# Optimization experiments

Hardware: AMD Instinct MI355X
Metric: run time of the kernel (lower is better)

Reference implementation:

```python
import jax, jax.numpy as jnp
import numpy as np

L, M, K, H, F, D = 8, 32768, 8, 128, 32, 3  # fronts, nodes/front, in-degree, hidden, feat, depth-branches


def _resnet(x, w1, b1, w2, b2, w3, b3):
    # resnet module: lay3(tanh(lay2(tanh(lay1(x)))) + x)
    h1 = jnp.tanh(x @ w1 + b1)
    h2 = jnp.tanh(h1 @ w2 + b2)
    return (h2 + x) @ w3 + b3


def setup_inputs() -> dict:
    key = jax.random.key(0)
    ks = iter(jax.random.split(key, 80))

    def nrm(shape, fan_in):
        return jax.random.normal(next(ks), shape, jnp.float32) / np.float32(np.sqrt(fan_in))

    def bias(shape):
        return 0.01 * jax.random.normal(next(ks), shape, jnp.float32)

    inp = {}
    inp["node_feats"] = jax.random.normal(next(ks), (L, M, F), jnp.float32)
    inp["pred_idx"] = jax.random.randint(next(ks), (L - 1, M, K), 0, M, jnp.int32)
    inp["embed_w"] = nrm((F, H), F); inp["embed_b"] = bias((H,))
    # d{1,2,3}_mp_bwd and d{1,2,3}_mp_bwd1 : per-depth pair of H-resnets, stacked [D,2,...]
    inp["mp_w1"] = nrm((D, 2, H, H), H); inp["mp_b1"] = bias((D, 2, H))
    inp["mp_w2"] = nrm((D, 2, H, H), H); inp["mp_b2"] = bias((D, 2, H))
    inp["mp_w3"] = nrm((D, 2, H, H), H); inp["mp_b3"] = bias((D, 2, H))
    for p in ("comb", "node"):  # d*_comb_embed(+1), d*_node_embeds(+1)
        inp[p + "_wide_w1"] = nrm((D, 2 * H, 2 * H), 2 * H); inp[p + "_wide_b1"] = bias((D, 2 * H))
        inp[p + "_wide_w2"] = nrm((D, 2 * H, 2 * H), 2 * H); inp[p + "_wide_b2"] = bias((D, 2 * H))
        inp[p + "_wide_w3"] = nrm((D, 2 * H, H), 2 * H);     inp[p + "_wide_b3"] = bias((D, H))
        inp[p + "_h_w1"] = nrm((D, H, H), H); inp[p + "_h_b1"] = bias((D, H))
        inp[p + "_h_w2"] = nrm((D, H, H), H); inp[p + "_h_b2"] = bias((D, H))
        inp[p + "_h_w3"] = nrm((D, H, H), H); inp[p + "_h_b3"] = bias((D, H))
    return inp


def reference(node_feats, pred_idx, embed_w, embed_b,
              mp_w1, mp_b1, mp_w2, mp_b2, mp_w3, mp_b3,
              comb_wide_w1, comb_wide_b1, comb_wide_w2, comb_wide_b2, comb_wide_w3, comb_wide_b3,
              comb_h_w1, comb_h_b1, comb_h_w2, comb_h_b2, comb_h_w3, comb_h_b3,
              node_wide_w1, node_wide_b1, node_wide_w2, node_wide_b2, node_wide_w3, node_wide_b3,
              node_h_w1, node_h_b1, node_h_w2, node_h_b2, node_h_w3, node_h_b3):
    # front 0 (topological roots): apply_func only -> tanh(embed_op(feats))
    e = jnp.tanh(node_feats[0] @ embed_w + embed_b)          # [M, H]
    outs = [e]
    prev = e
    for l in range(1, L):
        d = min(l - 1, 2)                                    # bwd_depth branch (d1/d2/d3)
        # msg_func + redux_func: gather mailbox from predecessor front, sum-reduce, MLP
        s = prev[pred_idx[l - 1]].sum(axis=1)                # [M, K, H] -> [M, H]
        r = jnp.tanh(_resnet(s, mp_w1[d, 0], mp_b1[d, 0], mp_w2[d, 0], mp_b2[d, 0], mp_w3[d, 0], mp_b3[d, 0]))
        r = jnp.tanh(_resnet(r, mp_w1[d, 1], mp_b1[d, 1], mp_w2[d, 1], mp_b2[d, 1], mp_w3[d, 1], mp_b3[d, 1]))
        # apply_func: embed, comb branch (bwd_node_embeds is all-zero for not-yet-processed nodes),
        # then node_embeds branch on cat(embeds, msgs_redux)
        e = jnp.tanh(node_feats[l] @ embed_w + embed_b)
        c = jnp.concatenate([e, jnp.zeros_like(e)], axis=-1)  # [M, 2H]
        e = jnp.tanh(_resnet(c, comb_wide_w1[d], comb_wide_b1[d], comb_wide_w2[d], comb_wide_b2[d], comb_wide_w3[d], comb_wide_b3[d]))
        e = jnp.tanh(_resnet(e, comb_h_w1[d], comb_h_b1[d], comb_h_w2[d], comb_h_b2[d], comb_h_w3[d], comb_h_b3[d]))
        c2 = jnp.concatenate([e, r], axis=-1)                 # [M, 2H]
        e = jnp.tanh(_resnet(c2, node_wide_w1[d], node_wide_b1[d], node_wide_w2[d], node_wide_b2[d], node_wide_w3[d], node_wide_b3[d]))
        e = jnp.tanh(_resnet(e, node_h_w1[d], node_h_b1[d], node_h_w2[d], node_h_b2[d], node_h_w3[d], node_h_b3[d]))
        outs.append(e)
        prev = e
    return jnp.stack(outs)                                    # graph.ndata['bwd_node_embeds'] : [L, M, H]
```

## Files before the change

kernel.cpp:

```cpp
#include <hip/hip_runtime.h>
#include <hip/hip_bf16.h>

#define M_NODES 32768

using f16x8 = __attribute__((ext_vector_type(8))) _Float16;
using f16x4 = __attribute__((ext_vector_type(4))) _Float16;
using f32x4 = __attribute__((ext_vector_type(4))) float;
typedef unsigned short u16;
typedef unsigned int   u32;

__device__ __forceinline__ u16 f2h(float f){
  _Float16 h = (_Float16)f;
  return __builtin_bit_cast(u16, h);
}
__device__ __forceinline__ float h2f(u16 h){
  return (float)__builtin_bit_cast(_Float16, h);
}
__device__ __forceinline__ float tanh_fast(float x){
  float t = __builtin_amdgcn_exp2f(x * 2.8853900817779268f);
  return 1.0f - 2.0f * __builtin_amdgcn_rcpf(t + 1.0f);
}

struct PrepPtrs { const float* p[16]; };

__global__ void prep_kernel(PrepPtrs pp, u16* ws){
  const int Bc[16] = {1,6,6,6,3,3,3,3,3,3,3,3,3,3,3,3};
  const int Kc[16] = {32,128,128,128,256,256,256,128,128,128,256,256,256,128,128,128};
  const int Nc[16] = {128,128,128,128,256,256,128,128,128,128,256,256,128,128,128,128};
  const int tot = 1576960;
  for (int i = blockIdx.x*blockDim.x + threadIdx.x; i < tot; i += gridDim.x*blockDim.x){
    int e = i, s = 0;
    while (true){ int sz = Bc[s]*Kc[s]*Nc[s]; if (e < sz) break; e -= sz; ++s; }
    int K = Kc[s], N = Nc[s];
    int kn = K*N;
    int b = e / kn; int r2 = e - b*kn;
    int n = r2 / K; int k = r2 - n*K;
    float v = pp.p[s][(size_t)b*kn + (size_t)k*N + n];
    ws[i] = f2h(v);
  }
}

__global__ __launch_bounds__(256) void front0_kernel(const float* __restrict__ feats,
                                                     const float* __restrict__ ew,
                                                     const float* __restrict__ eb,
                                                     float* __restrict__ out){
  __shared__ float fl[2048];
  const int brow = blockIdx.x * 64;
  const float* f0 = feats + (size_t)brow*32;
#pragma unroll
  for (int it = 0; it < 2; ++it){
    int idx = threadIdx.x + it*256;
    *(float4*)(&fl[idx*4]) = *(const float4*)(f0 + idx*4);
  }
  __syncthreads();
  const int col = threadIdx.x & 127, rh = threadIdx.x >> 7;
  float w[32];
#pragma unroll
  for (int k = 0; k < 32; ++k) w[k] = ew[k*128 + col];
  const float bv = eb[col];
  for (int r = 0; r < 32; ++r){
    int row = rh*32 + r;
    float acc = bv;
#pragma unroll
    for (int k = 0; k < 32; ++k) acc += fl[row*32 + k] * w[k];
    out[(size_t)(brow + row)*128 + col] = tanh_fast(acc);
  }
}

template<int KLOOP, int N, int WS, int AMODE, int RESMODE, int OUTMODE, bool INPLACE>
__device__ __forceinline__ void mm_stage(const u16* inA, u16* outB, const u16* resB,
                                         const u16* __restrict__ wt,
                                         const float* __restrict__ bias,
                                         float* gout, int phase)
{
  const int tid  = threadIdx.x;
  const int lane = tid & 63, nq = tid >> 6;
  const int q = lane >> 4, c = lane & 15;
  constexpr int NT = N / 64;
  constexpr int NP = KLOOP / 32;
  const float* inAf = (const float*)inA;
  float*       outF = (float*)outB;
  const float* resF = (const float*)resB;
  const int msk = NP - 1;
  const int ph = phase & msk;

  const u16* wrow[NT];
#pragma unroll
  for (int j = 0; j < NT; ++j){
    int nt = nq*2 + (j & 1) + (j >> 1) * 8;
    wrow[j] = wt + (size_t)(nt*16 + c)*WS + q*8;
  }
  f16x8 breg[2][NT];
#pragma unroll
  for (int j = 0; j < NT; ++j) breg[0][j] = *(const f16x8*)(wrow[j] + ph*32);
#pragma unroll
  for (int j = 0; j < NT; ++j) breg[1][j] = *(const f16x8*)(wrow[j] + ((ph + 1) & msk)*32);

  f32x4 acc[4][NT];
#pragma unroll
  for (int m = 0; m < 4; ++m)
#pragma unroll
    for (int j = 0; j < NT; ++j) acc[m][j] = (f32x4){0.f,0.f,0.f,0.f};

#pragma unroll
  for (int kp = 0; kp < NP; ++kp){
    const int slot = kp & 1;
    const int kpp = (ph + kp) & msk;
    f16x8 bc[NT];
#pragma unroll
    for (int j = 0; j < NT; ++j) bc[j] = breg[slot][j];
    if (kp + 2 < NP){
      int kn = (ph + kp + 2) & msk;
#pragma unroll
      for (int j = 0; j < NT; ++j) breg[slot][j] = *(const f16x8*)(wrow[j] + kn*32);
    }
#pragma unroll
    for (int m = 0; m < 4; ++m){
      if (AMODE == 0){
        f16x8 af = *(const f16x8*)(&inA[(m*16 + c)*264 + kpp*32 + q*8]);
#pragma unroll
        for (int j = 0; j < NT; ++j)
          acc[m][j] = __builtin_amdgcn_mfma_f32_16x16x32_f16(bc[j], af, acc[m][j], 0, 0, 0);
      } else {
        const float* ap = inAf + (m*16 + c)*132 + kpp*32 + q*8;
        float4 x0 = *(const float4*)(ap);
        float4 x1 = *(const float4*)(ap + 4);
        float xs[8] = {x0.x,x0.y,x0.z,x0.w,x1.x,x1.y,x1.z,x1.w};
        f16x8 ah, al;
#pragma unroll
        for (int k = 0; k < 8; ++k){
          _Float16 hi = (_Float16)xs[k];
          ah[k] = hi;
          al[k] = (_Float16)(xs[k] - (float)hi);
        }
#pragma unroll
        for (int j = 0; j < NT; ++j){
          acc[m][j] = __builtin_amdgcn_mfma_f32_16x16x32_f16(bc[j], ah, acc[m][j], 0, 0, 0);
          acc[m][j] = __builtin_amdgcn_mfma_f32_16x16x32_f16(bc[j], al, acc[m][j], 0, 0, 0);
        }
      }
    }
  }
  if (INPLACE) __syncthreads();
#pragma unroll
  for (int j = 0; j < NT; ++j){
    int nt = nq*2 + (j & 1) + (j >> 1) * 8;
    int col0 = nt*16 + q*4;
    float4 bq = *(const float4*)(bias + col0);
    float bvv[4] = {bq.x, bq.y, bq.z, bq.w};
#pragma unroll
    for (int m = 0; m < 4; ++m){
      int row = m*16 + c;
      float v[4];
#pragma unroll
      for (int r = 0; r < 4; ++r) v[r] = tanh_fast(acc[m][j][r] + bvv[r]);
      if (RESMODE == 2 || (RESMODE == 1 && j < 2)){
        f16x4 rv = *(const f16x4*)(&resB[row*264 + col0]);
#pragma unroll
        for (int r = 0; r < 4; ++r) v[r] += (float)rv[r];
      } else if (RESMODE == 3){
        float4 rf = *(const float4*)(&resF[row*132 + col0]);
        v[0] += rf.x; v[1] += rf.y; v[2] += rf.z; v[3] += rf.w;
      }
      if (OUTMODE == 2){
        float4 o = {v[0], v[1], v[2], v[3]};
        *(float4*)(&gout[(size_t)row*128 + col0]) = o;
      } else if (OUTMODE == 1){
        float4 o = {v[0], v[1], v[2], v[3]};
        *(float4*)(&outF[row*132 + col0]) = o;
      } else {
        f16x4 h;
#pragma unroll
        for (int r = 0; r < 4; ++r) h[r] = (_Float16)v[r];
        *(f16x4*)(&outB[row*264 + col0]) = h;
      }
    }
  }
  __syncthreads();
}

__device__ __forceinline__ void embed_stage(const float* __restrict__ featsRow,
                                            u16* outB, const u16* __restrict__ wt,
                                            const float* __restrict__ bias)
{
  const int tid  = threadIdx.x;
  const int lane = tid & 63, nq = tid >> 6;
  const int q = lane >> 4, c = lane & 15;
  f16x8 bf[2];
#pragma unroll
  for (int j = 0; j < 2; ++j){
    int nt = nq*2 + j;
    bf[j] = *(const f16x8*)(wt + (nt*16 + c)*32 + q*8);
  }
  f32x4 acc[4][2];
#pragma unroll
  for (int m = 0; m < 4; ++m){ acc[m][0] = (f32x4){0,0,0,0}; acc[m][1] = (f32x4){0,0,0,0}; }
#pragma unroll
  for (int m = 0; m < 4; ++m){
    int row = m*16 + c;
    const float* fp = featsRow + (size_t)row*32 + q*8;
    float4 a0 = *(const float4*)(fp);
    float4 a1 = *(const float4*)(fp + 4);
    float xs[8] = {a0.x,a0.y,a0.z,a0.w,a1.x,a1.y,a1.z,a1.w};
    f16x8 ah, al;
#pragma unroll
    for (int k = 0; k < 8; ++k){
      _Float16 hi = (_Float16)xs[k];
      ah[k] = hi;
      al[k] = (_Float16)(xs[k] - (float)hi);
    }
#pragma unroll
    for (int j = 0; j < 2; ++j){
      acc[m][j] = __builtin_amdgcn_mfma_f32_16x16x32_f16(bf[j], ah, acc[m][j], 0, 0, 0);
      acc[m][j] = __builtin_amdgcn_mfma_f32_16x16x32_f16(bf[j], al, acc[m][j], 0, 0, 0);
    }
  }
#pragma unroll
  for (int j = 0; j < 2; ++j){
    int nt = nq*2 + j;
    int col0 = nt*16 + q*4;
    float4 bq = *(const float4*)(bias + col0);
    float bvv[4] = {bq.x, bq.y, bq.z, bq.w};
#pragma unroll
    for (int m = 0; m < 4; ++m){
      int row = m*16 + c;
      f16x4 h;
#pragma unroll
      for (int r = 0; r < 4; ++r) h[r] = (_Float16)tanh_fast(acc[m][j][r] + bvv[r]);
      *(f16x4*)(&outB[row*264 + col0]) = h;
    }
  }
  __syncthreads();
}

struct FrontArgs {
  const float* feats; const int* pred;
  const u16* ws;
  float* out;
  const float* embed_b;
  const float* mp_b1; const float* mp_b2; const float* mp_b3;
  const float* cw_b1; const float* cw_b2; const float* cw_b3;
  const float* ch_b1; const float* ch_b2; const float* ch_b3;
  const float* nw_b1; const float* nw_b2; const float* nw_b3;
  const float* nh_b1; const float* nh_b2; const float* nh_b3;
  int l, d;
};

__global__ __launch_bounds__(256, 2) void front_kernel(FrontArgs A)
{
  extern __shared__ u16 lds[];
  u16* P  = lds;
  u16* Q  = lds + 16896;
  const int brow = blockIdx.x * 64;
  const int d = A.d;
  const u16* ws = A.ws;
  const int ph = blockIdx.x;

  {
    float* Pf = (float*)P;
    const float* prev = A.out + (size_t)(A.l - 1) * M_NODES * 128;
    const int c4 = threadIdx.x & 31;
    const int r0 = threadIdx.x >> 5;
#pragma unroll
    for (int rr = 0; rr < 8; ++rr){
      int row = r0 + rr*8;
      const int* ip = A.pred + ((size_t)(A.l - 1) * M_NODES + brow + row) * 8;
      float sx=0.f, sy=0.f, sz=0.f, sw=0.f;
#pragma unroll
      for (int p = 0; p < 8; ++p){
        const float4 v = *(const float4*)(prev + (size_t)ip[p]*128 + c4*4);
        sx += v.x; sy += v.y; sz += v.z; sw += v.w;
      }
      float4 o = {sx, sy, sz, sw};
      *(float4*)(&Pf[row*132 + c4*4]) = o;
    }
  }
  __syncthreads();

  const int d0 = d*2, d1 = d*2 + 1;
  mm_stage<128,128,128, 1,0,0,false>(P, Q, nullptr, ws + 4096   + (size_t)d0*16384, A.mp_b1 + d0*128, nullptr, ph);
  mm_stage<128,128,128, 0,3,1,false>(Q, P, P,       ws + 102400 + (size_t)d0*16384, A.mp_b2 + d0*128, nullptr, ph);
  mm_stage<128,128,128, 1,0,0,false>(P, Q, nullptr, ws + 200704 + (size_t)d0*16384, A.mp_b3 + d0*128, nullptr, ph);
  mm_stage<128,128,128, 0,0,0,false>(Q, P, nullptr, ws + 4096   + (size_t)d1*16384, A.mp_b1 + d1*128, nullptr, ph);
  mm_stage<128,128,128, 0,2,1,true >(P, P, Q,       ws + 102400 + (size_t)d1*16384, A.mp_b2 + d1*128, nullptr, ph);
  mm_stage<128,128,128, 1,0,0,false>(P, Q + 128, nullptr, ws + 200704 + (size_t)d1*16384, A.mp_b3 + d1*128, nullptr, ph);
  embed_stage(A.feats + ((size_t)A.l * M_NODES + brow) * 32, Q, ws, A.embed_b);
  mm_stage<128,256,256, 0,0,0,false>(Q, P, nullptr, ws + 299008 + (size_t)d*65536, A.cw_b1 + d*256, nullptr, ph);
  mm_stage<256,256,256, 0,1,0,true >(P, P, Q,       ws + 495616 + (size_t)d*65536, A.cw_b2 + d*256, nullptr, ph);
  mm_stage<256,128,256, 0,0,0,false>(P, Q, nullptr, ws + 692224 + (size_t)d*32768, A.cw_b3 + d*128, nullptr, ph);
  mm_stage<128,128,128, 0,0,0,false>(Q, P, nullptr, ws + 790528 + (size_t)d*16384, A.ch_b1 + d*128, nullptr, ph);
  mm_stage<128,128,128, 0,2,0,true >(P, P, Q,       ws + 839680 + (size_t)d*16384, A.ch_b2 + d*128, nullptr, ph);
  mm_stage<128,128,128, 0,0,0,false>(P, Q, nullptr, ws + 888832 + (size_t)d*16384, A.ch_b3 + d*128, nullptr, ph);
  mm_stage<256,256,256, 0,0,0,false>(Q, P, nullptr, ws + 937984  + (size_t)d*65536, A.nw_b1 + d*256, nullptr, ph);
  mm_stage<256,256,256, 0,2,0,true >(P, P, Q,       ws + 1134592 + (size_t)d*65536, A.nw_b2 + d*256, nullptr, ph);
  mm_stage<256,128,256, 0,0,0,false>(P, Q, nullptr, ws + 1331200 + (size_t)d*32768, A.nw_b3 + d*128, nullptr, ph);
  mm_stage<128,128,128, 0,0,0,false>(Q, P, nullptr, ws + 1429504 + (size_t)d*16384, A.nh_b1 + d*128, nullptr, ph);
  mm_stage<128,128,128, 0,2,0,true >(P, P, Q,       ws + 1478656 + (size_t)d*16384, A.nh_b2 + d*128, nullptr, ph);
  float* gout = A.out + ((size_t)A.l * M_NODES + brow) * 128;
  mm_stage<128,128,128, 0,0,2,false>(P, nullptr, nullptr, ws + 1527808 + (size_t)d*16384, A.nh_b3 + d*128, gout, ph);
}

extern "C" void kernel_launch(void* const* d_in, const int* in_sizes, int n_in,
                              void* d_out, int out_size, void* d_ws, size_t ws_size,
                              hipStream_t stream)
{
  (void)in_sizes; (void)n_in; (void)out_size; (void)ws_size;
  const float* feats = (const float*)d_in[0];
  const int*   pred  = (const int*)d_in[1];
  u16*   ws  = (u16*)d_ws;
  float* out = (float*)d_out;

  PrepPtrs pp;
  const int wIdx[16] = {2,4,6,8,10,12,14,16,18,20,22,24,26,28,30,32};
  for (int i = 0; i < 16; ++i) pp.p[i] = (const float*)d_in[wIdx[i]];
  prep_kernel<<<2048, 256, 0, stream>>>(pp, ws);

  front0_kernel<<<M_NODES/64, 256, 0, stream>>>(feats, (const float*)d_in[2], (const float*)d_in[3], out);

  const size_t LDSB = (size_t)(2*64*264) * sizeof(u16);
  (void)hipFuncSetAttribute((const void*)front_kernel,
                            hipFuncAttributeMaxDynamicSharedMemorySize, (int)LDSB);

  FrontArgs A;
  A.feats = feats; A.pred = pred; A.ws = ws; A.out = out;
  A.embed_b = (const float*)d_in[3];
  A.mp_b1 = (const float*)d_in[5];  A.mp_b2 = (const float*)d_in[7];  A.mp_b3 = (const float*)d_in[9];
  A.cw_b1 = (const float*)d_in[11]; A.cw_b2 = (const float*)d_in[13]; A.cw_b3 = (const float*)d_in[15];
  A.ch_b1 = (const float*)d_in[17]; A.ch_b2 = (const float*)d_in[19]; A.ch_b3 = (const float*)d_in[21];
  A.nw_b1 = (const float*)d_in[23]; A.nw_b2 = (const float*)d_in[25]; A.nw_b3 = (const float*)d_in[27];
  A.nh_b1 = (const float*)d_in[29]; A.nh_b2 = (const float*)d_in[31]; A.nh_b3 = (const float*)d_in[33];

  for (int l = 1; l < 8; ++l){
    A.l = l;
    A.d = (l - 1 < 2) ? (l - 1) : 2;
    front_kernel<<<M_NODES/64, 256, LDSB, stream>>>(A);
  }
}
```

Measured before the change: 662.7 us.

## Double threads per block to eight waves, halving per-wave column tiles

Each 64-row tile in front_kernel is now processed by 512 threads instead of 256. Every wave owns half as many 16-column N-tiles in each matmul stage and in the embed stage, and the gather loop covers rows with a stride of 16. The goal is more waves per CU to hide latency, with fewer accumulator registers per thread. The cost is that each weight fragment is loaded by more waves, each wave does less MFMA work between barriers, and the __launch_bounds__(512,4) request may not be met given the LDS use of about 67KB per block.

New measurement: 679.4 us. 2.5% more time.

```diff
diff --git a/kernel.cpp b/kernel.cpp
--- a/kernel.cpp
+++ b/kernel.cpp
@@ -76,7 +76,7 @@
   const int tid  = threadIdx.x;
   const int lane = tid & 63, nq = tid >> 6;
   const int q = lane >> 4, c = lane & 15;
-  constexpr int NT = N / 64;
+  constexpr int NT = N / 128;
   constexpr int NP = KLOOP / 32;
   const float* inAf = (const float*)inA;
   float*       outF = (float*)outB;
@@ -87,7 +87,7 @@
   const u16* wrow[NT];
 #pragma unroll
   for (int j = 0; j < NT; ++j){
-    int nt = nq*2 + (j & 1) + (j >> 1) * 8;
+    int nt = nq + j*8;
     wrow[j] = wt + (size_t)(nt*16 + c)*WS + q*8;
   }
   f16x8 breg[2][NT];
@@ -144,7 +144,7 @@
   if (INPLACE) __syncthreads();
 #pragma unroll
   for (int j = 0; j < NT; ++j){
-    int nt = nq*2 + (j & 1) + (j >> 1) * 8;
+    int nt = nq + j*8;
     int col0 = nt*16 + q*4;
     float4 bq = *(const float4*)(bias + col0);
     float bvv[4] = {bq.x, bq.y, bq.z, bq.w};
@@ -154,7 +154,7 @@
       float v[4];
 #pragma unroll
       for (int r = 0; r < 4; ++r) v[r] = tanh_fast(acc[m][j][r] + bvv[r]);
-      if (RESMODE == 2 || (RESMODE == 1 && j < 2)){
+      if (RESMODE == 2 || (RESMODE == 1 && j == 0)){
         f16x4 rv = *(const f16x4*)(&resB[row*264 + col0]);
 #pragma unroll
         for (int r = 0; r < 4; ++r) v[r] += (float)rv[r];
@@ -186,15 +186,10 @@
   const int tid  = threadIdx.x;
   const int lane = tid & 63, nq = tid >> 6;
   const int q = lane >> 4, c = lane & 15;
-  f16x8 bf[2];
-#pragma unroll
-  for (int j = 0; j < 2; ++j){
-    int nt = nq*2 + j;
-    bf[j] = *(const f16x8*)(wt + (nt*16 + c)*32 + q*8);
-  }
-  f32x4 acc[4][2];
-#pragma unroll
-  for (int m = 0; m < 4; ++m){ acc[m][0] = (f32x4){0,0,0,0}; acc[m][1] = (f32x4){0,0,0,0}; }
+  f16x8 bf = *(const f16x8*)(wt + (nq*16 + c)*32 + q*8);
+  f32x4 acc[4];
+#pragma unroll
+  for (int m = 0; m < 4; ++m) acc[m] = (f32x4){0,0,0,0};
 #pragma unroll
   for (int m = 0; m < 4; ++m){
     int row = m*16 + c;
@@ -209,26 +204,19 @@
       ah[k] = hi;
       al[k] = (_Float16)(xs[k] - (float)hi);
     }
-#pragma unroll
-    for (int j = 0; j < 2; ++j){
-      acc[m][j] = __builtin_amdgcn_mfma_f32_16x16x32_f16(bf[j], ah, acc[m][j], 0, 0, 0);
-      acc[m][j] = __builtin_amdgcn_mfma_f32_16x16x32_f16(bf[j], al, acc[m][j], 0, 0, 0);
-    }
-  }
-#pragma unroll
-  for (int j = 0; j < 2; ++j){
-    int nt = nq*2 + j;
-    int col0 = nt*16 + q*4;
-    float4 bq = *(const float4*)(bias + col0);
-    float bvv[4] = {bq.x, bq.y, bq.z, bq.w};
-#pragma unroll
-    for (int m = 0; m < 4; ++m){
-      int row = m*16 + c;
-      f16x4 h;
-#pragma unroll
-      for (int r = 0; r < 4; ++r) h[r] = (_Float16)tanh_fast(acc[m][j][r] + bvv[r]);
-      *(f16x4*)(&outB[row*264 + col0]) = h;
-    }
+    acc[m] = __builtin_amdgcn_mfma_f32_16x16x32_f16(bf, ah, acc[m], 0, 0, 0);
+    acc[m] = __builtin_amdgcn_mfma_f32_16x16x32_f16(bf, al, acc[m], 0, 0, 0);
+  }
+  int col0 = nq*16 + q*4;
+  float4 bq = *(const float4*)(bias + col0);
+  float bvv[4] = {bq.x, bq.y, bq.z, bq.w};
+#pragma unroll
+  for (int m = 0; m < 4; ++m){
+    int row = m*16 + c;
+    f16x4 h;
+#pragma unroll
+    for (int r = 0; r < 4; ++r) h[r] = (_Float16)tanh_fast(acc[m][r] + bvv[r]);
+    *(f16x4*)(&outB[row*264 + col0]) = h;
   }
   __syncthreads();
 }
@@ -246,7 +234,7 @@
   int l, d;
 };
 
-__global__ __launch_bounds__(256, 2) void front_kernel(FrontArgs A)
+__global__ __launch_bounds__(512, 4) void front_kernel(FrontArgs A)
 {
   extern __shared__ u16 lds[];
   u16* P  = lds;
@@ -262,8 +250,8 @@
     const int c4 = threadIdx.x & 31;
     const int r0 = threadIdx.x >> 5;
 #pragma unroll
-    for (int rr = 0; rr < 8; ++rr){
-      int row = r0 + rr*8;
+    for (int rr = 0; rr < 4; ++rr){
+      int row = r0 + rr*16;
       const int* ip = A.pred + ((size_t)(A.l - 1) * M_NODES + brow + row) * 8;
       float sx=0.f, sy=0.f, sz=0.f, sw=0.f;
 #pragma unroll
@@ -333,6 +321,6 @@
   for (int l = 1; l < 8; ++l){
     A.l = l;
     A.d = (l - 1 < 2) ? (l - 1) : 2;
-    front_kernel<<<M_NODES/64, 256, LDSB, stream>>>(A);
-  }
-}
+    front_kernel<<<M_NODES/64, 512, LDSB, stream>>>(A);
+  }
+}
```

## Prefetch next stage's weight fragments during current stage epilogue; burst-load A fragments

Applied to the files above, without the earlier changes.

Introduces a two-slot weight register ring so each GEMM stage issues the first global weight loads of the next stage right after its MFMA loop, overlapping them with the tanh/bias epilogue and the barrier. This hides the global-load latency at the start of each of the chained stages. For 128-K fp16-input stages, it also loads all 16 A fragments from LDS up front instead of inside the k-loop. Register pressure rises, which risks spills or lower occupancy.

Measured after the change: 645.1 us, median of 2. 2.7% less time.

```diff
diff --git a/kernel.cpp b/kernel.cpp
--- a/kernel.cpp
+++ b/kernel.cpp
@@ -9,16 +9,16 @@
 typedef unsigned short u16;
 typedef unsigned int   u32;
 
+__device__ __forceinline__ float h2f(u16 h){
+  return (float)__builtin_bit_cast(_Float16, h);
+}
+__device__ __forceinline__ float tanh_fast(float x){
+  float t = __builtin_amdgcn_exp2f(x * 2.8853900817779268f);
+  return 1.0f - 2.0f * __builtin_amdgcn_rcpf(t + 1.0f);
+}
 __device__ __forceinline__ u16 f2h(float f){
   _Float16 h = (_Float16)f;
   return __builtin_bit_cast(u16, h);
-}
-__device__ __forceinline__ float h2f(u16 h){
-  return (float)__builtin_bit_cast(_Float16, h);
-}
-__device__ __forceinline__ float tanh_fast(float x){
-  float t = __builtin_amdgcn_exp2f(x * 2.8853900817779268f);
-  return 1.0f - 2.0f * __builtin_amdgcn_rcpf(t + 1.0f);
 }
 
 struct PrepPtrs { const float* p[16]; };
@@ -67,57 +67,93 @@
   }
 }
 
-template<int KLOOP, int N, int WS, int AMODE, int RESMODE, int OUTMODE, bool INPLACE>
+struct WRing {
+  const u16* wrow[4];
+  f16x8 b0[4], b1[4];
+};
+
+template<int N, int WS, int NP>
+__device__ __forceinline__ void wpreload(WRing& R, const u16* __restrict__ wt, int phase){
+  const int tid  = threadIdx.x;
+  const int lane = tid & 63, nq = tid >> 6;
+  const int q = lane >> 4, c = lane & 15;
+  constexpr int NT = N / 64;
+  const int msk = NP - 1;
+  const int p0 = phase & msk, p1 = (phase + 1) & msk;
+#pragma unroll
+  for (int j = 0; j < NT; ++j){
+    int nt = nq*2 + (j & 1) + (j >> 1) * 8;
+    R.wrow[j] = wt + (size_t)(nt*16 + c)*WS + q*8;
+  }
+#pragma unroll
+  for (int j = 0; j < NT; ++j) R.b0[j] = *(const f16x8*)(R.wrow[j] + p0*32);
+#pragma unroll
+  for (int j = 0; j < NT; ++j) R.b1[j] = *(const f16x8*)(R.wrow[j] + p1*32);
+}
+
+template<int KLOOP, int N, int WS, int AMODE, int RESMODE, int OUTMODE, bool INPLACE,
+         int NN, int NWS, int NNP>
 __device__ __forceinline__ void mm_stage(const u16* inA, u16* outB, const u16* resB,
-                                         const u16* __restrict__ wt,
-                                         const float* __restrict__ bias,
-                                         float* gout, int phase)
+                                         const float* __restrict__ bias, float* gout,
+                                         int phase, WRing& cur, WRing& nxt,
+                                         const u16* __restrict__ wtnext)
 {
   const int tid  = threadIdx.x;
   const int lane = tid & 63, nq = tid >> 6;
   const int q = lane >> 4, c = lane & 15;
   constexpr int NT = N / 64;
   constexpr int NP = KLOOP / 32;
+  constexpr bool ABURST = (AMODE == 0 && NP == 4);
   const float* inAf = (const float*)inA;
   float*       outF = (float*)outB;
   const float* resF = (const float*)resB;
   const int msk = NP - 1;
   const int ph = phase & msk;
 
-  const u16* wrow[NT];
-#pragma unroll
-  for (int j = 0; j < NT; ++j){
-    int nt = nq*2 + (j & 1) + (j >> 1) * 8;
-    wrow[j] = wt + (size_t)(nt*16 + c)*WS + q*8;
-  }
-  f16x8 breg[2][NT];
-#pragma unroll
-  for (int j = 0; j < NT; ++j) breg[0][j] = *(const f16x8*)(wrow[j] + ph*32);
-#pragma unroll
-  for (int j = 0; j < NT; ++j) breg[1][j] = *(const f16x8*)(wrow[j] + ((ph + 1) & msk)*32);
-
   f32x4 acc[4][NT];
 #pragma unroll
   for (int m = 0; m < 4; ++m)
 #pragma unroll
     for (int j = 0; j < NT; ++j) acc[m][j] = (f32x4){0.f,0.f,0.f,0.f};
 
+  f16x8 aall[ABURST ? 16 : 1];
+  if (ABURST){
+#pragma unroll
+    for (int kp = 0; kp < 4; ++kp){
+      int kpp = (ph + kp) & 3;
+#pragma unroll
+      for (int m = 0; m < 4; ++m)
+        aall[kp*4 + m] = *(const f16x8*)(&inA[(m*16 + c)*264 + kpp*32 + q*8]);
+    }
+  }
+
 #pragma unroll
   for (int kp = 0; kp < NP; ++kp){
-    const int slot = kp & 1;
     const int kpp = (ph + kp) & msk;
     f16x8 bc[NT];
-#pragma unroll
-    for (int j = 0; j < NT; ++j) bc[j] = breg[slot][j];
+    if ((kp & 1) == 0){
+#pragma unroll
+      for (int j = 0; j < NT; ++j) bc[j] = cur.b0[j];
+    } else {
+#pragma unroll
+      for (int j = 0; j < NT; ++j) bc[j] = cur.b1[j];
+    }
     if (kp + 2 < NP){
       int kn = (ph + kp + 2) & msk;
-#pragma unroll
-      for (int j = 0; j < NT; ++j) breg[slot][j] = *(const f16x8*)(wrow[j] + kn*32);
+      if ((kp & 1) == 0){
+#pragma unroll
+        for (int j = 0; j < NT; ++j) cur.b0[j] = *(const f16x8*)(cur.wrow[j] + kn*32);
+      } else {
+#pragma unroll
+        for (int j = 0; j < NT; ++j) cur.b1[j] = *(const f16x8*)(cur.wrow[j] + kn*32);
+      }
     }
 #pragma unroll
     for (int m = 0; m < 4; ++m){
       if (AMODE == 0){
-        f16x8 af = *(const f16x8*)(&inA[(m*16 + c)*264 + kpp*32 + q*8]);
+        f16x8 af;
+        if (ABURST) af = aall[kp*4 + m];
+        else        af = *(const f16x8*)(&inA[(m*16 + c)*264 + kpp*32 + q*8]);
 #pragma unroll
         for (int j = 0; j < NT; ++j)
           acc[m][j] = __builtin_amdgcn_mfma_f32_16x16x32_f16(bc[j], af, acc[m][j], 0, 0, 0);
@@ -141,6 +177,7 @@
       }
     }
   }
+  if constexpr (NN > 0) wpreload<NN, NWS, NNP>(nxt, wtnext, phase);
   if (INPLACE) __syncthreads();
 #pragma unroll
   for (int j = 0; j < NT; ++j){
@@ -180,18 +217,13 @@
 }
 
 __device__ __forceinline__ void embed_stage(const float* __restrict__ featsRow,
-                                            u16* outB, const u16* __restrict__ wt,
-                                            const float* __restrict__ bias)
+                                            u16* outB, const float* __restrict__ bias,
+                                            int phase, WRing& cur, WRing& nxt,
+                                            const u16* __restrict__ wtnext)
 {
   const int tid  = threadIdx.x;
   const int lane = tid & 63, nq = tid >> 6;
   const int q = lane >> 4, c = lane & 15;
-  f16x8 bf[2];
-#pragma unroll
-  for (int j = 0; j < 2; ++j){
-    int nt = nq*2 + j;
-    bf[j] = *(const f16x8*)(wt + (nt*16 + c)*32 + q*8);
-  }
   f32x4 acc[4][2];
 #pragma unroll
   for (int m = 0; m < 4; ++m){ acc[m][0] = (f32x4){0,0,0,0}; acc[m][1] = (f32x4){0,0,0,0}; }
@@ -211,10 +243,11 @@
     }
 #pragma unroll
     for (int j = 0; j < 2; ++j){
-      acc[m][j] = __builtin_amdgcn_mfma_f32_16x16x32_f16(bf[j], ah, acc[m][j], 0, 0, 0);
-      acc[m][j] = __builtin_amdgcn_mfma_f32_16x16x32_f16(bf[j], al, acc[m][j], 0, 0, 0);
-    }
-  }
+      acc[m][j] = __builtin_amdgcn_mfma_f32_16x16x32_f16(cur.b0[j], ah, acc[m][j], 0, 0, 0);
+      acc[m][j] = __builtin_amdgcn_mfma_f32_16x16x32_f16(cur.b0[j], al, acc[m][j], 0, 0, 0);
+    }
+  }
+  wpreload<256, 256, 4>(nxt, wtnext, phase);
 #pragma unroll
   for (int j = 0; j < 2; ++j){
     int nt = nq*2 + j;
@@ -255,6 +288,10 @@
   const int d = A.d;
   const u16* ws = A.ws;
   const int ph = blockIdx.x;
+  const int d0 = d*2, d1 = d*2 + 1;
+
+  WRing rA, rB;
+  wpreload<128, 128, 4>(rA, ws + 4096 + (size_t)d0*16384, ph);
 
   {
     float* Pf = (float*)P;
@@ -277,27 +314,26 @@
   }
   __syncthreads();
 
-  const int d0 = d*2, d1 = d*2 + 1;
-  mm_stage<128,128,128, 1,0,0,false>(P, Q, nullptr, ws + 4096   + (size_t)d0*16384, A.mp_b1 + d0*128, nullptr, ph);
-  mm_stage<128,128,128, 0,3,1,false>(Q, P, P,       ws + 102400 + (size_t)d0*16384, A.mp_b2 + d0*128, nullptr, ph);
-  mm_stage<128,128,128, 1,0,0,false>(P, Q, nullptr, ws + 200704 + (size_t)d0*16384, A.mp_b3 + d0*128, nullptr, ph);
-  mm_stage<128,128,128, 0,0,0,false>(Q, P, nullptr, ws + 4096   + (size_t)d1*16384, A.mp_b1 + d1*128, nullptr, ph);
-  mm_stage<128,128,128, 0,2,1,true >(P, P, Q,       ws + 102400 + (size_t)d1*16384, A.mp_b2 + d1*128, nullptr, ph);
-  mm_stage<128,128,128, 1,0,0,false>(P, Q + 128, nullptr, ws + 200704 + (size_t)d1*16384, A.mp_b3 + d1*128, nullptr, ph);
-  embed_stage(A.feats + ((size_t)A.l * M_NODES + brow) * 32, Q, ws, A.embed_b);
-  mm_stage<128,256,256, 0,0,0,false>(Q, P, nullptr, ws + 299008 + (size_t)d*65536, A.cw_b1 + d*256, nullptr, ph);
-  mm_stage<256,256,256, 0,1,0,true >(P, P, Q,       ws + 495616 + (size_t)d*65536, A.cw_b2 + d*256, nullptr, ph);
-  mm_stage<256,128,256, 0,0,0,false>(P, Q, nullptr, ws + 692224 + (size_t)d*32768, A.cw_b3 + d*128, nullptr, ph);
-  mm_stage<128,128,128, 0,0,0,false>(Q, P, nullptr, ws + 790528 + (size_t)d*16384, A.ch_b1 + d*128, nullptr, ph);
-  mm_stage<128,128,128, 0,2,0,true >(P, P, Q,       ws + 839680 + (size_t)d*16384, A.ch_b2 + d*128, nullptr, ph);
-  mm_stage<128,128,128, 0,0,0,false>(P, Q, nullptr, ws + 888832 + (size_t)d*16384, A.ch_b3 + d*128, nullptr, ph);
-  mm_stage<256,256,256, 0,0,0,false>(Q, P, nullptr, ws + 937984  + (size_t)d*65536, A.nw_b1 + d*256, nullptr, ph);
-  mm_stage<256,256,256, 0,2,0,true >(P, P, Q,       ws + 1134592 + (size_t)d*65536, A.nw_b2 + d*256, nullptr, ph);
-  mm_stage<256,128,256, 0,0,0,false>(P, Q, nullptr, ws + 1331200 + (size_t)d*32768, A.nw_b3 + d*128, nullptr, ph);
-  mm_stage<128,128,128, 0,0,0,false>(Q, P, nullptr, ws + 1429504 + (size_t)d*16384, A.nh_b1 + d*128, nullptr, ph);
-  mm_stage<128,128,128, 0,2,0,true >(P, P, Q,       ws + 1478656 + (size_t)d*16384, A.nh_b2 + d*128, nullptr, ph);
+  mm_stage<128,128,128, 1,0,0,false, 128,128,4>(P, Q, nullptr, A.mp_b1 + d0*128, nullptr, ph, rA, rB, ws + 102400 + (size_t)d0*16384);
+  mm_stage<128,128,128, 0,3,1,false, 128,128,4>(Q, P, P, A.mp_b2 + d0*128, nullptr, ph, rB, rA, ws + 200704 + (size_t)d0*16384);
+  mm_stage<128,128,128, 1,0,0,false, 128,128,4>(P, Q, nullptr, A.mp_b3 + d0*128, nullptr, ph, rA, rB, ws + 4096 + (size_t)d1*16384);
+  mm_stage<128,128,128, 0,0,0,false, 128,128,4>(Q, P, nullptr, A.mp_b1 + d1*128, nullptr, ph, rB, rA, ws + 102400 + (size_t)d1*16384);
+  mm_stage<128,128,128, 0,2,1,true , 128,128,4>(P, P, Q, A.mp_b2 + d1*128, nullptr, ph, rA, rB, ws + 200704 + (size_t)d1*16384);
+  mm_stage<128,128,128, 1,0,0,false, 128,32,1>(P, Q + 128, nullptr, A.mp_b3 + d1*128, nullptr, ph, rB, rA, ws);
+  embed_stage(A.feats + ((size_t)A.l * M_NODES + brow) * 32, Q, A.embed_b, ph, rA, rB, ws + 299008 + (size_t)d*65536);
+  mm_stage<128,256,256, 0,0,0,false, 256,256,8>(Q, P, nullptr, A.cw_b1 + d*256, nullptr, ph, rB, rA, ws + 495616 + (size_t)d*65536);
+  mm_stage<256,256,256, 0,1,0,true , 128,256,8>(P, P, Q, A.cw_b2 + d*256, nullptr, ph, rA, rB, ws + 692224 + (size_t)d*32768);
+  mm_stage<256,128,256, 0,0,0,false, 128,128,4>(P, Q, nullptr, A.cw_b3 + d*128, nullptr, ph, rB, rA, ws + 790528 + (size_t)d*16384);
+  mm_stage<128,128,128, 0,0,0,false, 128,128,4>(Q, P, nullptr, A.ch_b1 + d*128, nullptr, ph, rA, rB, ws + 839680 + (size_t)d*16384);
+  mm_stage<128,128,128, 0,2,0,true , 128,128,4>(P, P, Q, A.ch_b2 + d*128, nullptr, ph, rB, rA, ws + 888832 + (size_t)d*16384);
+  mm_stage<128,128,128, 0,0,0,false, 256,256,8>(P, Q, nullptr, A.ch_b3 + d*128, nullptr, ph, rA, rB, ws + 937984 + (size_t)d*65536);
+  mm_stage<256,256,256, 0,0,0,false, 256,256,8>(Q, P, nullptr, A.nw_b1 + d*256, nullptr, ph, rB, rA, ws + 1134592 + (size_t)d*65536);
+  mm_stage<256,256,256, 0,2,0,true , 128,256,8>(P, P, Q, A.nw_b2 + d*256, nullptr, ph, rA, rB, ws + 1331200 + (size_t)d*32768);
+  mm_stage<256,128,256, 0,0,0,false, 128,128,4>(P, Q, nullptr, A.nw_b3 + d*128, nullptr, ph, rB, rA, ws + 1429504 + (size_t)d*16384);
+  mm_stage<128,128,128, 0,0,0,false, 128,128,4>(Q, P, nullptr, A.nh_b1 + d*128, nullptr, ph, rA, rB, ws + 1478656 + (size_t)d*16384);
+  mm_stage<128,128,128, 0,2,0,true , 128,128,4>(P, P, Q, A.nh_b2 + d*128, nullptr, ph, rB, rA, ws + 1527808 + (size_t)d*16384);
   float* gout = A.out + ((size_t)A.l * M_NODES + brow) * 128;
-  mm_stage<128,128,128, 0,0,2,false>(P, nullptr, nullptr, ws + 1527808 + (size_t)d*16384, A.nh_b3 + d*128, gout, ph);
+  mm_stage<128,128,128, 0,0,2,false, 0,0,1>(P, nullptr, nullptr, A.nh_b3 + d*128, gout, ph, rA, rB, nullptr);
 }
 
 extern "C" void kernel_launch(void* const* d_in, const int* in_sizes, int n_in,
```
